# Performance work log

Hardware: AMD Instinct MI355X
Metric: run time of the kernel (lower is better)

## Reference

```python
import jax, jax.numpy as jnp
import numpy as np

B = 4096      # batch
D_IN = 512    # input_dim
D = 256       # d_model
T = 424       # n_targets
L = 6         # num_layers
EPS = 1e-5    # torch LayerNorm default


def _ln(x, g, b):
    m = jnp.mean(x, axis=-1, keepdims=True)
    v = jnp.var(x, axis=-1, keepdims=True)
    return (x - m) * jax.lax.rsqrt(v + EPS) * g + b


def setup_inputs() -> dict:
    key = jax.random.key(0)
    ks = iter(jax.random.split(key, 32))
    r = lambda shape, s=0.05: jax.random.normal(next(ks), shape, dtype=jnp.float32) * s
    return {
        'x': jax.random.normal(next(ks), (B, D_IN), dtype=jnp.float32),
        'proj_W': r((4, D // 4, D_IN)), 'proj_b': r((4, D // 4)),
        'attn_in_W': r((L, 3 * D, D)), 'attn_in_b': r((L, 3 * D)),
        'attn_out_W': r((L, D, D)), 'attn_out_b': r((L, D)),
        'ln_g': jnp.ones((L, D), jnp.float32), 'ln_b': jnp.zeros((L, D), jnp.float32),
        'ff_W1': r((L, 4 * D, D)), 'ff_b1': r((L, 4 * D)),
        'ff_W2': r((L, D, 4 * D)), 'ff_b2': r((L, D)),
        'cross_in_W': r((3 * D, D)), 'cross_in_b': r((3 * D,)),
        'cross_out_W': r((D, D)), 'cross_out_b': r((D,)),
        'tp_W1': r((T, D // 2, D)), 'tp_b1': r((T, D // 2)),
        'tp_ln_g': jnp.ones((T, D // 2), jnp.float32), 'tp_ln_b': jnp.zeros((T, D // 2), jnp.float32),
        'tp_W2': r((T, D // 4, D // 2)), 'tp_b2': r((T, D // 4)),
        'tp_W3': r((T, D // 4)), 'tp_b3': r((T,)),
    }


def reference(x, proj_W, proj_b, attn_in_W, attn_in_b, attn_out_W, attn_out_b,
              ln_g, ln_b, ff_W1, ff_b1, ff_W2, ff_b2,
              cross_in_W, cross_in_b, cross_out_W, cross_out_b,
              tp_W1, tp_b1, tp_ln_g, tp_ln_b, tp_W2, tp_b2, tp_W3, tp_b3):
    # 4 feature projections -> concat == reshape of stacked einsum  [B, 4, D/4] -> [B, D]
    h = jnp.einsum('bd,pkd->bpk', x, proj_W) + proj_b
    h = h.reshape(h.shape[0], D)

    # 6 transformer blocks on seq_len=1: softmax over a single key == 1, so
    # MHA(x,x,x) reduces exactly to out_proj(v_proj(x)); dropout = identity (eval).
    for i in range(L):
        Wv, bv = attn_in_W[i, 2 * D:], attn_in_b[i, 2 * D:]
        attn = (h @ Wv.T + bv) @ attn_out_W[i].T + attn_out_b[i]
        h = _ln(h + attn, ln_g[i], ln_b[i])          # same norm instance reused
        ff = jax.nn.gelu(h @ ff_W1[i].T + ff_b1[i], approximate=False) @ ff_W2[i].T + ff_b2[i]
        h = _ln(h + ff, ln_g[i], ln_b[i])

    # cross-target attention, also seq_len=1 -> v/out projections only
    Wv, bv = cross_in_W[2 * D:], cross_in_b[2 * D:]
    h = h + ((h @ Wv.T + bv) @ cross_out_W.T + cross_out_b)

    # 424 per-target MLP heads, batched as grouped GEMMs
    t = jnp.einsum('bd,tkd->btk', h, tp_W1) + tp_b1          # [B, T, 128]
    t = jax.nn.relu(_ln(t, tp_ln_g, tp_ln_b))
    t = jax.nn.relu(jnp.einsum('btk,tmk->btm', t, tp_W2) + tp_b2)  # [B, T, 64]
    out = jnp.einsum('btm,tm->bt', t, tp_W3) + tp_b3         # [B, T]
    return out
```

## Files before the change

### kernel.cpp

```cpp
#include <hip/hip_runtime.h>
#include <stdint.h>
#include <utility>
#include <type_traits>

using bf16x8 = __attribute__((ext_vector_type(8))) short;
using f32x4  = __attribute__((ext_vector_type(4))) float;

__device__ __forceinline__ f32x4 mfma16(bf16x8 a, bf16x8 b, f32x4 c) {
  return __builtin_amdgcn_mfma_f32_16x16x32_bf16(a, b, c, 0, 0, 0);
}

__device__ __forceinline__ unsigned short f2b_rne(float f) {
  union { float f; unsigned u; } v; v.f = f;
  unsigned r = v.u + 0x7fffu + ((v.u >> 16) & 1u);
  return (unsigned short)(r >> 16);
}

__device__ __forceinline__ void gload16(const void* g, void* l) {
  __builtin_amdgcn_global_load_lds(
      (const __attribute__((address_space(1))) void*)g,
      (__attribute__((address_space(3))) void*)l, 16, 0, 0);
}

template<int N> __device__ __forceinline__ void vmwait() {
  if constexpr (N <= 0)      asm volatile("s_waitcnt vmcnt(0)" ::: "memory");
  else if constexpr (N == 4) asm volatile("s_waitcnt vmcnt(4)" ::: "memory");
  else                       asm volatile("s_waitcnt vmcnt(8)" ::: "memory");
}

template<class F, int... Is>
__device__ __forceinline__ void sfor_impl(F&& f, std::integer_sequence<int, Is...>) {
  (f(std::integral_constant<int, Is>{}), ...);
}
template<int N, class F>
__device__ __forceinline__ void sfor(F&& f) {
  sfor_impl(static_cast<F&&>(f), std::make_integer_sequence<int, N>{});
}

__device__ __forceinline__ void stage_tile(const unsigned short* __restrict__ W, int K,
                                           int col0, int kt, char* slot, int lane) {
#pragma unroll
  for (int i = 0; i < 4; ++i) {
    const int chunk = i * 64 + lane;
    const int ci = chunk >> 4, kc = chunk & 15;
    const unsigned short* src = W + (size_t)(col0 + ci) * K + kt * 128
                                + (((kc * 16) ^ ((ci & 7) << 4)) >> 1);
    gload16(src, slot + i * 1024);
  }
}

template<int NCG, int NKT, int AS, int K>
__device__ __forceinline__ void gemm_pipe(const unsigned short* __restrict__ W, int c0,
                                          const char* __restrict__ abuf,
                                          char* __restrict__ ring, int lane,
                                          f32x4 (&acc)[NCG]) {
  const int r = lane & 15, hi16 = (lane >> 4) << 4;
  const int swz = (r & 7) << 4;
  constexpr int TILES = NCG * NKT;
  stage_tile(W, K, c0, 0, ring, lane);
  if constexpr (TILES > 1)
    stage_tile(W, K, c0 + (1 % NCG) * 16, 1 / NCG, ring + 4096, lane);
  bf16x8 areg[4];
  sfor<TILES>([&](auto tc) {
    constexpr int t = tc.value;
    constexpr int kt = t / NCG, cg = t % NCG;
    vmwait<((t + 2 <= TILES) ? 4 : 0)>();
    __builtin_amdgcn_sched_barrier(0);
    if constexpr (t + 2 < TILES) {
      constexpr int t2 = t + 2;
      stage_tile(W, K, c0 + (t2 % NCG) * 16, t2 / NCG, ring + (t2 % 3) * 4096, lane);
    }
    const char* slot = ring + (t % 3) * 4096;
#pragma unroll
    for (int ksl = 0; ksl < 4; ++ksl) {
      if constexpr (cg == 0)
        areg[ksl] = *reinterpret_cast<const bf16x8*>(
            abuf + r * AS + ((kt * 256 + ksl * 64 + hi16) ^ swz));
      const bf16x8 b = *reinterpret_cast<const bf16x8*>(
          slot + r * 256 + ((ksl * 64 + hi16) ^ swz));
      acc[cg] = mfma16(areg[ksl], b, acc[cg]);
    }
  });
}

__global__ void f2b_kernel(const float* __restrict__ s, unsigned short* __restrict__ d, int n4) {
  int i = blockIdx.x * 256 + threadIdx.x;
  if (i >= n4) return;
  float4 v = reinterpret_cast<const float4*>(s)[i];
  ushort4 o;
  o.x = f2b_rne(v.x); o.y = f2b_rne(v.y); o.z = f2b_rne(v.z); o.w = f2b_rne(v.w);
  reinterpret_cast<ushort4*>(d)[i] = o;
}

__global__ __launch_bounds__(256) void compose_attn(
    const float* __restrict__ aiW, const float* __restrict__ aib,
    const float* __restrict__ aoW, const float* __restrict__ aob,
    const float* __restrict__ ciW, const float* __restrict__ cib,
    const float* __restrict__ coW, const float* __restrict__ cob,
    unsigned short* __restrict__ wEff, float* __restrict__ bEff) {
  const int mat = blockIdx.y;
  const float* Wo = (mat < 6) ? aoW + (size_t)mat * 65536 : coW;
  const float* Wv = (mat < 6) ? aiW + (size_t)mat * 196608 + 131072 : ciW + 131072;
  const float* bv = (mat < 6) ? aib + mat * 768 + 512 : cib + 512;
  const float* bo = (mat < 6) ? aob + mat * 256 : cob;
  unsigned short* Wd = wEff + (size_t)mat * 65536;
  const int m = blockIdx.x * 16 + (threadIdx.x >> 4);
  const int k0 = (threadIdx.x & 15) * 16;
  float c[16] = {};
  for (int j = 0; j < 256; ++j) {
    const float a = Wo[m * 256 + j];
    const float* Br = Wv + j * 256 + k0;
#pragma unroll
    for (int kk = 0; kk < 16; ++kk) c[kk] = fmaf(a, Br[kk], c[kk]);
  }
#pragma unroll
  for (int kk = 0; kk < 16; ++kk) Wd[m * 256 + k0 + kk] = f2b_rne(c[kk]);
  if (blockIdx.x == 0) {
    const int mm = threadIdx.x;
    float s = 0.f;
    for (int j = 0; j < 256; ++j) s = fmaf(Wo[mm * 256 + j], bv[j], s);
    bEff[mat * 256 + mm] = s + bo[mm];
  }
}

__global__ __launch_bounds__(512, 2) void trunk_fused(
    const unsigned short* __restrict__ xb, const unsigned short* __restrict__ pWb,
    const float* __restrict__ projb,
    const unsigned short* __restrict__ wEff, const float* __restrict__ bEff,
    const unsigned short* __restrict__ f1Wb, const float* __restrict__ f1b,
    const unsigned short* __restrict__ f2Wb, const float* __restrict__ f2bp,
    const float* __restrict__ lng, const float* __restrict__ lnb,
    unsigned short* __restrict__ hbf) {
  __shared__ char hbuf[16 * 512];
  __shared__ char gbuf[16 * 2048];
  __shared__ char ringbuf[8 * 12288];
  __shared__ float red[2][16][8];
  const int tid = threadIdx.x, wid = tid >> 6, lane = tid & 63;
  const int r = lane & 15, hi = lane >> 4;
  const int swz = (r & 7) << 4;
  const int row0 = blockIdx.x << 4;
  const int colb = wid * 32;
  char* ring = ringbuf + wid * 12288;

#pragma unroll
  for (int i = 0; i < 2; ++i) {
    const int id = tid + i * 512, row = id >> 6, c8 = id & 63;
    bf16x8 v = *reinterpret_cast<const bf16x8*>(xb + (size_t)(row0 + row) * 512 + c8 * 8);
    *reinterpret_cast<bf16x8*>(gbuf + row * 1024 + ((c8 * 16) ^ ((row & 7) << 4))) = v;
  }
  __syncthreads();

  f32x4 hreg[2];

  auto store_hb = [&]() {
#pragma unroll
    for (int cf = 0; cf < 2; ++cf) {
      const int cb = (colb + cf * 16 + r) * 2;
#pragma unroll
      for (int j = 0; j < 4; ++j) {
        const int row = hi * 4 + j;
        *reinterpret_cast<unsigned short*>(hbuf + row * 512 + (cb ^ ((row & 7) << 4))) =
            f2b_rne(hreg[cf][j]);
      }
    }
  };

  auto ln_apply = [&](float gm0, float gm1, float bb0, float bb1) {
    float sum[4], sq[4];
#pragma unroll
    for (int j = 0; j < 4; ++j) {
      const float v0 = hreg[0][j], v1 = hreg[1][j];
      sum[j] = v0 + v1; sq[j] = v0 * v0 + v1 * v1;
    }
#pragma unroll
    for (int m = 1; m < 16; m <<= 1)
#pragma unroll
      for (int j = 0; j < 4; ++j) {
        sum[j] += __shfl_xor(sum[j], m, 64);
        sq[j]  += __shfl_xor(sq[j],  m, 64);
      }
    if (r == 0)
#pragma unroll
      for (int j = 0; j < 4; ++j) {
        red[0][hi * 4 + j][wid] = sum[j];
        red[1][hi * 4 + j][wid] = sq[j];
      }
    __syncthreads();
#pragma unroll
    for (int j = 0; j < 4; ++j) {
      const int row = hi * 4 + j;
      f32x4 p0 = *reinterpret_cast<const f32x4*>(&red[0][row][0]);
      f32x4 p1 = *reinterpret_cast<const f32x4*>(&red[0][row][4]);
      f32x4 q0 = *reinterpret_cast<const f32x4*>(&red[1][row][0]);
      f32x4 q1 = *reinterpret_cast<const f32x4*>(&red[1][row][4]);
      const float ts = p0[0]+p0[1]+p0[2]+p0[3]+p1[0]+p1[1]+p1[2]+p1[3];
      const float tq = q0[0]+q0[1]+q0[2]+q0[3]+q1[0]+q1[1]+q1[2]+q1[3];
      const float mean = ts * (1.f / 256.f);
      const float rstd = rsqrtf(tq * (1.f / 256.f) - mean * mean + 1e-5f);
      hreg[0][j] = (hreg[0][j] - mean) * rstd * gm0 + bb0;
      hreg[1][j] = (hreg[1][j] - mean) * rstd * gm1 + bb1;
    }
  };

  {
    f32x4 acc[2] = {};
    gemm_pipe<2, 4, 1024, 512>(pWb, colb, gbuf, ring, lane, acc);
    const float bv0 = projb[colb + r], bv1 = projb[colb + 16 + r];
#pragma unroll
    for (int j = 0; j < 4; ++j) { hreg[0][j] = acc[0][j] + bv0; hreg[1][j] = acc[1][j] + bv1; }
  }
  store_hb();
  __syncthreads();

  for (int L = 0; L < 6; ++L) {
    const float gm0 = lng[L * 256 + colb + r],      gm1 = lng[L * 256 + colb + 16 + r];
    const float bb0 = lnb[L * 256 + colb + r],      bb1 = lnb[L * 256 + colb + 16 + r];
    {
      f32x4 acc[2] = {};
      gemm_pipe<2, 2, 512, 256>(wEff + (size_t)L * 65536, colb, hbuf, ring, lane, acc);
      const float be0 = bEff[L * 256 + colb + r], be1 = bEff[L * 256 + colb + 16 + r];
#pragma unroll
      for (int j = 0; j < 4; ++j) { hreg[0][j] += acc[0][j] + be0; hreg[1][j] += acc[1][j] + be1; }
    }
    ln_apply(gm0, gm1, bb0, bb1);
    store_hb();
    __syncthreads();
    {
      f32x4 accf[8] = {};
      gemm_pipe<8, 2, 512, 256>(f1Wb + (size_t)L * 262144, wid * 128, hbuf, ring, lane, accf);
#pragma unroll
      for (int cf = 0; cf < 8; ++cf) {
        const int colw = wid * 128 + cf * 16 + r;
        const float bv = f1b[L * 1024 + colw];
        const int cb = colw * 2;
#pragma unroll
        for (int j = 0; j < 4; ++j) {
          float y = accf[cf][j] + bv;
          y = 0.5f * y * (1.f + erff(y * 0.70710678118654752f));
          const int row = hi * 4 + j;
          *reinterpret_cast<unsigned short*>(gbuf + row * 2048 + (cb ^ ((row & 7) << 4))) = f2b_rne(y);
        }
      }
    }
    __syncthreads();
    {
      f32x4 acc[2] = {};
      gemm_pipe<2, 8, 2048, 1024>(f2Wb + (size_t)L * 262144, colb, gbuf, ring, lane, acc);
      const float be0 = f2bp[L * 256 + colb + r], be1 = f2bp[L * 256 + colb + 16 + r];
#pragma unroll
      for (int j = 0; j < 4; ++j) { hreg[0][j] += acc[0][j] + be0; hreg[1][j] += acc[1][j] + be1; }
    }
    ln_apply(gm0, gm1, bb0, bb1);
    store_hb();
    __syncthreads();
  }

  {
    f32x4 acc[2] = {};
    gemm_pipe<2, 2, 512, 256>(wEff + 6ull * 65536, colb, hbuf, ring, lane, acc);
    const float be0 = bEff[1536 + colb + r], be1 = bEff[1536 + colb + 16 + r];
#pragma unroll
    for (int j = 0; j < 4; ++j) { hreg[0][j] += acc[0][j] + be0; hreg[1][j] += acc[1][j] + be1; }
  }
#pragma unroll
  for (int cf = 0; cf < 2; ++cf)
#pragma unroll
    for (int j = 0; j < 4; ++j)
      hbf[(size_t)(row0 + hi * 4 + j) * 256 + colb + cf * 16 + r] = f2b_rne(hreg[cf][j]);
}

__global__ __launch_bounds__(512, 2) void phase_d2(
    const unsigned short* __restrict__ hbf, const unsigned short* __restrict__ w1b,
    const float* __restrict__ b1, const float* __restrict__ lng, const float* __restrict__ lnb,
    const unsigned short* __restrict__ w2b, const float* __restrict__ b2,
    const float* __restrict__ w3, const float* __restrict__ b3,
    float* __restrict__ out) {
  __shared__ char sm[149504];
  const int tid = threadIdx.x, wid = tid >> 6, lane = tid & 63;
  const int r = lane & 15, hi = lane >> 4;
  const int sw = (r & 7) << 4;
  const int t = blockIdx.y;

  const unsigned short* w1t = w1b + (size_t)t * 32768;
  const unsigned short* w2t = w2b + (size_t)t * 8192;
#pragma unroll
  for (int i = 0; i < 8; ++i) {
    const int id = tid + i * 512;
    const int c = id >> 5, s = id & 31;
    bf16x8 v = *reinterpret_cast<const bf16x8*>(w1t + c * 256 + s * 8);
    *reinterpret_cast<bf16x8*>(sm + c * 512 + ((s * 16) ^ ((c & 7) << 4))) = v;
  }
#pragma unroll
  for (int i = 0; i < 2; ++i) {
    const int id = tid + i * 512;
    const int c = id >> 4, s = id & 15;
    bf16x8 v = *reinterpret_cast<const bf16x8*>(w2t + c * 128 + s * 8);
    *reinterpret_cast<bf16x8*>(sm + 65536 + c * 256 + ((s * 16) ^ ((c & 7) << 4))) = v;
  }
  {
    float v;
    if (tid < 128)      v = b1 [t * 128 + tid];
    else if (tid < 256) v = lng[t * 128 + tid - 128];
    else if (tid < 384) v = lnb[t * 128 + tid - 256];
    else if (tid < 448) v = b2 [t * 64  + tid - 384];
    else                v = w3 [t * 64  + tid - 448];
    reinterpret_cast<float*>(sm + 81920)[tid] = v;
  }
  __syncthreads();

  const float* cb1 = reinterpret_cast<const float*>(sm + 81920);
  const float* cg  = cb1 + 128;
  const float* cbe = cb1 + 256;
  const float* cb2 = cb1 + 384;
  const float* cw3 = cb1 + 448;
  char* t1w = sm + 83968 + wid * 8192;
  const float b3t = b3[t];
  const int token_b0 = blockIdx.x * 1024;

  for (int tile = 0; tile < 2; ++tile) {
    const int B0 = token_b0 + tile * 512 + wid * 64;

    f32x4 acc1[8][4] = {};
    bf16x8 bc[4], bn[4];
#pragma unroll
    for (int bf = 0; bf < 4; ++bf)
      bc[bf] = *reinterpret_cast<const bf16x8*>(hbf + (size_t)(B0 + bf * 16 + r) * 256 + hi * 8);
#pragma unroll
    for (int ks = 0; ks < 8; ++ks) {
      bf16x8 a[8];
#pragma unroll
      for (int cf = 0; cf < 8; ++cf)
        a[cf] = *reinterpret_cast<const bf16x8*>(sm + (cf * 16 + r) * 512 + ((ks * 64 + hi * 16) ^ sw));
      if (ks < 7) {
#pragma unroll
        for (int bf = 0; bf < 4; ++bf)
          bn[bf] = *reinterpret_cast<const bf16x8*>(hbf + (size_t)(B0 + bf * 16 + r) * 256 + (ks + 1) * 32 + hi * 8);
      }
#pragma unroll
      for (int cf = 0; cf < 8; ++cf)
#pragma unroll
        for (int bf = 0; bf < 4; ++bf)
          acc1[cf][bf] = mfma16(a[cf], bc[bf], acc1[cf][bf]);
#pragma unroll
      for (int bf = 0; bf < 4; ++bf) bc[bf] = bn[bf];
    }

#pragma unroll
    for (int cf = 0; cf < 8; ++cf) {
      f32x4 b1v = *reinterpret_cast<const f32x4*>(cb1 + cf * 16 + hi * 4);
#pragma unroll
      for (int bf = 0; bf < 4; ++bf) acc1[cf][bf] += b1v;
    }

    float mu[4], rsd[4];
#pragma unroll
    for (int bf = 0; bf < 4; ++bf) {
      float s = 0.f, s2 = 0.f;
#pragma unroll
      for (int cf = 0; cf < 8; ++cf)
#pragma unroll
        for (int j = 0; j < 4; ++j) { float v = acc1[cf][bf][j]; s += v; s2 += v * v; }
      s  += __shfl_xor(s, 16, 64);  s  += __shfl_xor(s, 32, 64);
      s2 += __shfl_xor(s2, 16, 64); s2 += __shfl_xor(s2, 32, 64);
      const float m = s * (1.f / 128.f);
      mu[bf] = m;
      rsd[bf] = rsqrtf(s2 * (1.f / 128.f) - m * m + 1e-5f);
    }

    f32x4 acc2[4][4] = {};
#pragma unroll
    for (int half = 0; half < 2; ++half) {
#pragma unroll
      for (int cf = 0; cf < 8; ++cf) {
        f32x4 gv = *reinterpret_cast<const f32x4*>(cg  + cf * 16 + hi * 4);
        f32x4 bv = *reinterpret_cast<const f32x4*>(cbe + cf * 16 + hi * 4);
#pragma unroll
        for (int bl = 0; bl < 2; ++bl) {
          const int bf = half * 2 + bl;
          unsigned o01, o23;
          {
            float y0 = fmaxf((acc1[cf][bf][0] - mu[bf]) * rsd[bf] * gv[0] + bv[0], 0.f);
            float y1 = fmaxf((acc1[cf][bf][1] - mu[bf]) * rsd[bf] * gv[1] + bv[1], 0.f);
            float y2 = fmaxf((acc1[cf][bf][2] - mu[bf]) * rsd[bf] * gv[2] + bv[2], 0.f);
            float y3 = fmaxf((acc1[cf][bf][3] - mu[bf]) * rsd[bf] * gv[3] + bv[3], 0.f);
            o01 = (unsigned)f2b_rne(y0) | ((unsigned)f2b_rne(y1) << 16);
            o23 = (unsigned)f2b_rne(y2) | ((unsigned)f2b_rne(y3) << 16);
          }
          uint2 pk; pk.x = o01; pk.y = o23;
          *reinterpret_cast<uint2*>(t1w + (bl * 16 + r) * 256 + ((cf * 32 + hi * 8) ^ sw)) = pk;
        }
      }
#pragma unroll
      for (int ks = 0; ks < 4; ++ks) {
        bf16x8 a2[4];
#pragma unroll
        for (int cf2 = 0; cf2 < 4; ++cf2)
          a2[cf2] = *reinterpret_cast<const bf16x8*>(sm + 65536 + (cf2 * 16 + r) * 256 + ((ks * 64 + hi * 16) ^ sw));
#pragma unroll
        for (int bl = 0; bl < 2; ++bl) {
          bf16x8 bb = *reinterpret_cast<const bf16x8*>(t1w + (bl * 16 + r) * 256 + ((ks * 64 + hi * 16) ^ sw));
#pragma unroll
          for (int cf2 = 0; cf2 < 4; ++cf2)
            acc2[cf2][half * 2 + bl] = mfma16(a2[cf2], bb, acc2[cf2][half * 2 + bl]);
        }
      }
    }

    float s[4] = {0.f, 0.f, 0.f, 0.f};
#pragma unroll
    for (int cf2 = 0; cf2 < 4; ++cf2) {
      f32x4 b2v = *reinterpret_cast<const f32x4*>(cb2 + cf2 * 16 + hi * 4);
      f32x4 w3v = *reinterpret_cast<const f32x4*>(cw3 + cf2 * 16 + hi * 4);
#pragma unroll
      for (int bf = 0; bf < 4; ++bf)
#pragma unroll
        for (int j = 0; j < 4; ++j)
          s[bf] += fmaxf(acc2[cf2][bf][j] + b2v[j], 0.f) * w3v[j];
    }
#pragma unroll
    for (int bf = 0; bf < 4; ++bf) {
      s[bf] += __shfl_xor(s[bf], 16, 64);
      s[bf] += __shfl_xor(s[bf], 32, 64);
      if (hi == 0) out[(size_t)(B0 + bf * 16 + r) * 424 + t] = s[bf] + b3t;
    }
  }
}

extern "C" void kernel_launch(void* const* d_in, const int* in_sizes, int n_in,
                              void* d_out, int out_size, void* d_ws, size_t ws_size,
                              hipStream_t stream) {
  const float* x     = (const float*)d_in[0];
  const float* projW = (const float*)d_in[1];
  const float* projb = (const float*)d_in[2];
  const float* aiW   = (const float*)d_in[3];
  const float* aib   = (const float*)d_in[4];
  const float* aoW   = (const float*)d_in[5];
  const float* aob   = (const float*)d_in[6];
  const float* lng   = (const float*)d_in[7];
  const float* lnbp  = (const float*)d_in[8];
  const float* f1W   = (const float*)d_in[9];
  const float* f1b   = (const float*)d_in[10];
  const float* f2W   = (const float*)d_in[11];
  const float* f2bp  = (const float*)d_in[12];
  const float* ciW   = (const float*)d_in[13];
  const float* cib   = (const float*)d_in[14];
  const float* coW   = (const float*)d_in[15];
  const float* cob   = (const float*)d_in[16];
  const float* tpW1  = (const float*)d_in[17];
  const float* tpb1  = (const float*)d_in[18];
  const float* tplng = (const float*)d_in[19];
  const float* tplnb = (const float*)d_in[20];
  const float* tpW2  = (const float*)d_in[21];
  const float* tpb2  = (const float*)d_in[22];
  const float* tpW3  = (const float*)d_in[23];
  const float* tpb3  = (const float*)d_in[24];
  float* out = (float*)d_out;

  char* ws = (char*)d_ws;
  size_t off = 0;
  auto alloc = [&](size_t n) { char* p = ws + off; off = (off + n + 255) & ~(size_t)255; return p; };
  unsigned short* xb   = (unsigned short*)alloc(4096ull * 512 * 2);
  unsigned short* pWb  = (unsigned short*)alloc(256ull * 512 * 2);
  unsigned short* f1Wb = (unsigned short*)alloc(6ull * 1024 * 256 * 2);
  unsigned short* f2Wb = (unsigned short*)alloc(6ull * 256 * 1024 * 2);
  unsigned short* W1b  = (unsigned short*)alloc(424ull * 128 * 256 * 2);
  unsigned short* W2b  = (unsigned short*)alloc(424ull * 64 * 128 * 2);
  unsigned short* wEff = (unsigned short*)alloc(7ull * 256 * 256 * 2);
  float*          bEff = (float*)alloc(7ull * 256 * 4);
  unsigned short* hbf  = (unsigned short*)alloc(4096ull * 256 * 2);

  auto conv = [&](const float* s, unsigned short* d, size_t n) {
    int n4 = (int)(n >> 2);
    f2b_kernel<<<dim3((n4 + 255) / 256), dim3(256), 0, stream>>>(s, d, n4);
  };
  compose_attn<<<dim3(16, 7), dim3(256), 0, stream>>>(aiW, aib, aoW, aob, ciW, cib, coW, cob, wEff, bEff);
  conv(x, xb, 4096ull * 512);
  conv(projW, pWb, 256ull * 512);
  conv(f1W, f1Wb, 6ull * 1024 * 256);
  conv(f2W, f2Wb, 6ull * 256 * 1024);
  conv(tpW1, W1b, 424ull * 128 * 256);
  conv(tpW2, W2b, 424ull * 64 * 128);

  trunk_fused<<<dim3(256), dim3(512), 0, stream>>>(
      xb, pWb, projb, wEff, bEff, f1Wb, f1b, f2Wb, f2bp, lng, lnbp, hbf);

  phase_d2<<<dim3(4, 424), dim3(512), 0, stream>>>(hbf, W1b, tpb1, tplng, tplnb, W2b, tpb2, tpW3, tpb3, out);
}
```

Baseline: 523.6 us.

## Shrink head kernel LDS/tiles, exchange LN output via shuffles, raise occupancy

The per-target head kernel now gives each workgroup 256 tokens (32 per wave) instead of 1024, over a 1D grid of 6784 blocks laid out so consecutive blocks pair up on the same target. The LDS staging of W2 and of the per-wave t1 scratch is dropped. The second GEMM's B fragments are rebuilt with cross-lane shuffles from packed registers, and W2, b2 and w3 are read directly from global memory. This lowers shared memory to about 67KB and launch bounds to 4 blocks per CU to raise occupancy. The cost is that W1 is reloaded into LDS four times more often per target, and there are more shuffle instructions.

```diff
diff --git a/kernel.cpp b/kernel.cpp
--- a/kernel.cpp
+++ b/kernel.cpp
@@ -5,6 +5,7 @@
 
 using bf16x8 = __attribute__((ext_vector_type(8))) short;
 using f32x4  = __attribute__((ext_vector_type(4))) float;
+using u32x4  = __attribute__((ext_vector_type(4))) unsigned;
 
 __device__ __forceinline__ f32x4 mfma16(bf16x8 a, bf16x8 b, f32x4 c) {
   return __builtin_amdgcn_mfma_f32_16x16x32_bf16(a, b, c, 0, 0, 0);
@@ -137,7 +138,6 @@
   __shared__ float red[2][16][8];
   const int tid = threadIdx.x, wid = tid >> 6, lane = tid & 63;
   const int r = lane & 15, hi = lane >> 4;
-  const int swz = (r & 7) << 4;
   const int row0 = blockIdx.x << 4;
   const int colb = wid * 32;
   char* ring = ringbuf + wid * 12288;
@@ -269,20 +269,24 @@
       hbf[(size_t)(row0 + hi * 4 + j) * 256 + colb + cf * 16 + r] = f2b_rne(hreg[cf][j]);
 }
 
-__global__ __launch_bounds__(512, 2) void phase_d2(
+__global__ __launch_bounds__(512, 4) void phase_d4(
     const unsigned short* __restrict__ hbf, const unsigned short* __restrict__ w1b,
     const float* __restrict__ b1, const float* __restrict__ lng, const float* __restrict__ lnb,
     const unsigned short* __restrict__ w2b, const float* __restrict__ b2,
     const float* __restrict__ w3, const float* __restrict__ b3,
     float* __restrict__ out) {
-  __shared__ char sm[149504];
+  __shared__ char sm[65536 + 1536];
   const int tid = threadIdx.x, wid = tid >> 6, lane = tid & 63;
   const int r = lane & 15, hi = lane >> 4;
   const int sw = (r & 7) << 4;
-  const int t = blockIdx.y;
+
+  const int wg = blockIdx.x;
+  const int pp = wg / 848, rem = wg % 848;
+  const int t = rem >> 1;
+  const int part = pp * 2 + (rem & 1);
+  const int B0 = part * 256 + wid * 32;
 
   const unsigned short* w1t = w1b + (size_t)t * 32768;
-  const unsigned short* w2t = w2b + (size_t)t * 8192;
 #pragma unroll
   for (int i = 0; i < 8; ++i) {
     const int id = tid + i * 512;
@@ -290,40 +294,24 @@
     bf16x8 v = *reinterpret_cast<const bf16x8*>(w1t + c * 256 + s * 8);
     *reinterpret_cast<bf16x8*>(sm + c * 512 + ((s * 16) ^ ((c & 7) << 4))) = v;
   }
-#pragma unroll
-  for (int i = 0; i < 2; ++i) {
-    const int id = tid + i * 512;
-    const int c = id >> 4, s = id & 15;
-    bf16x8 v = *reinterpret_cast<const bf16x8*>(w2t + c * 128 + s * 8);
-    *reinterpret_cast<bf16x8*>(sm + 65536 + c * 256 + ((s * 16) ^ ((c & 7) << 4))) = v;
-  }
-  {
+  if (tid < 384) {
     float v;
     if (tid < 128)      v = b1 [t * 128 + tid];
     else if (tid < 256) v = lng[t * 128 + tid - 128];
-    else if (tid < 384) v = lnb[t * 128 + tid - 256];
-    else if (tid < 448) v = b2 [t * 64  + tid - 384];
-    else                v = w3 [t * 64  + tid - 448];
-    reinterpret_cast<float*>(sm + 81920)[tid] = v;
+    else                v = lnb[t * 128 + tid - 256];
+    reinterpret_cast<float*>(sm + 65536)[tid] = v;
   }
   __syncthreads();
 
-  const float* cb1 = reinterpret_cast<const float*>(sm + 81920);
+  const float* cb1 = reinterpret_cast<const float*>(sm + 65536);
   const float* cg  = cb1 + 128;
   const float* cbe = cb1 + 256;
-  const float* cb2 = cb1 + 384;
-  const float* cw3 = cb1 + 448;
-  char* t1w = sm + 83968 + wid * 8192;
-  const float b3t = b3[t];
-  const int token_b0 = blockIdx.x * 1024;
-
-  for (int tile = 0; tile < 2; ++tile) {
-    const int B0 = token_b0 + tile * 512 + wid * 64;
-
-    f32x4 acc1[8][4] = {};
-    bf16x8 bc[4], bn[4];
-#pragma unroll
-    for (int bf = 0; bf < 4; ++bf)
+
+  f32x4 acc1[8][2] = {};
+  {
+    bf16x8 bc[2], bn[2];
+#pragma unroll
+    for (int bf = 0; bf < 2; ++bf)
       bc[bf] = *reinterpret_cast<const bf16x8*>(hbf + (size_t)(B0 + bf * 16 + r) * 256 + hi * 8);
 #pragma unroll
     for (int ks = 0; ks < 8; ++ks) {
@@ -333,96 +321,108 @@
         a[cf] = *reinterpret_cast<const bf16x8*>(sm + (cf * 16 + r) * 512 + ((ks * 64 + hi * 16) ^ sw));
       if (ks < 7) {
 #pragma unroll
-        for (int bf = 0; bf < 4; ++bf)
+        for (int bf = 0; bf < 2; ++bf)
           bn[bf] = *reinterpret_cast<const bf16x8*>(hbf + (size_t)(B0 + bf * 16 + r) * 256 + (ks + 1) * 32 + hi * 8);
       }
 #pragma unroll
       for (int cf = 0; cf < 8; ++cf)
 #pragma unroll
-        for (int bf = 0; bf < 4; ++bf)
+        for (int bf = 0; bf < 2; ++bf)
           acc1[cf][bf] = mfma16(a[cf], bc[bf], acc1[cf][bf]);
 #pragma unroll
-      for (int bf = 0; bf < 4; ++bf) bc[bf] = bn[bf];
-    }
-
-#pragma unroll
-    for (int cf = 0; cf < 8; ++cf) {
-      f32x4 b1v = *reinterpret_cast<const f32x4*>(cb1 + cf * 16 + hi * 4);
-#pragma unroll
-      for (int bf = 0; bf < 4; ++bf) acc1[cf][bf] += b1v;
-    }
-
-    float mu[4], rsd[4];
-#pragma unroll
-    for (int bf = 0; bf < 4; ++bf) {
-      float s = 0.f, s2 = 0.f;
-#pragma unroll
-      for (int cf = 0; cf < 8; ++cf)
-#pragma unroll
-        for (int j = 0; j < 4; ++j) { float v = acc1[cf][bf][j]; s += v; s2 += v * v; }
-      s  += __shfl_xor(s, 16, 64);  s  += __shfl_xor(s, 32, 64);
-      s2 += __shfl_xor(s2, 16, 64); s2 += __shfl_xor(s2, 32, 64);
-      const float m = s * (1.f / 128.f);
-      mu[bf] = m;
-      rsd[bf] = rsqrtf(s2 * (1.f / 128.f) - m * m + 1e-5f);
-    }
-
-    f32x4 acc2[4][4] = {};
-#pragma unroll
-    for (int half = 0; half < 2; ++half) {
-#pragma unroll
-      for (int cf = 0; cf < 8; ++cf) {
-        f32x4 gv = *reinterpret_cast<const f32x4*>(cg  + cf * 16 + hi * 4);
-        f32x4 bv = *reinterpret_cast<const f32x4*>(cbe + cf * 16 + hi * 4);
-#pragma unroll
-        for (int bl = 0; bl < 2; ++bl) {
-          const int bf = half * 2 + bl;
-          unsigned o01, o23;
-          {
-            float y0 = fmaxf((acc1[cf][bf][0] - mu[bf]) * rsd[bf] * gv[0] + bv[0], 0.f);
-            float y1 = fmaxf((acc1[cf][bf][1] - mu[bf]) * rsd[bf] * gv[1] + bv[1], 0.f);
-            float y2 = fmaxf((acc1[cf][bf][2] - mu[bf]) * rsd[bf] * gv[2] + bv[2], 0.f);
-            float y3 = fmaxf((acc1[cf][bf][3] - mu[bf]) * rsd[bf] * gv[3] + bv[3], 0.f);
-            o01 = (unsigned)f2b_rne(y0) | ((unsigned)f2b_rne(y1) << 16);
-            o23 = (unsigned)f2b_rne(y2) | ((unsigned)f2b_rne(y3) << 16);
-          }
-          uint2 pk; pk.x = o01; pk.y = o23;
-          *reinterpret_cast<uint2*>(t1w + (bl * 16 + r) * 256 + ((cf * 32 + hi * 8) ^ sw)) = pk;
-        }
-      }
-#pragma unroll
-      for (int ks = 0; ks < 4; ++ks) {
-        bf16x8 a2[4];
-#pragma unroll
-        for (int cf2 = 0; cf2 < 4; ++cf2)
-          a2[cf2] = *reinterpret_cast<const bf16x8*>(sm + 65536 + (cf2 * 16 + r) * 256 + ((ks * 64 + hi * 16) ^ sw));
-#pragma unroll
-        for (int bl = 0; bl < 2; ++bl) {
-          bf16x8 bb = *reinterpret_cast<const bf16x8*>(t1w + (bl * 16 + r) * 256 + ((ks * 64 + hi * 16) ^ sw));
-#pragma unroll
-          for (int cf2 = 0; cf2 < 4; ++cf2)
-            acc2[cf2][half * 2 + bl] = mfma16(a2[cf2], bb, acc2[cf2][half * 2 + bl]);
-        }
-      }
-    }
-
-    float s[4] = {0.f, 0.f, 0.f, 0.f};
-#pragma unroll
-    for (int cf2 = 0; cf2 < 4; ++cf2) {
-      f32x4 b2v = *reinterpret_cast<const f32x4*>(cb2 + cf2 * 16 + hi * 4);
-      f32x4 w3v = *reinterpret_cast<const f32x4*>(cw3 + cf2 * 16 + hi * 4);
-#pragma unroll
-      for (int bf = 0; bf < 4; ++bf)
-#pragma unroll
-        for (int j = 0; j < 4; ++j)
-          s[bf] += fmaxf(acc2[cf2][bf][j] + b2v[j], 0.f) * w3v[j];
-    }
-#pragma unroll
-    for (int bf = 0; bf < 4; ++bf) {
-      s[bf] += __shfl_xor(s[bf], 16, 64);
-      s[bf] += __shfl_xor(s[bf], 32, 64);
-      if (hi == 0) out[(size_t)(B0 + bf * 16 + r) * 424 + t] = s[bf] + b3t;
-    }
+      for (int bf = 0; bf < 2; ++bf) bc[bf] = bn[bf];
+    }
+  }
+
+#pragma unroll
+  for (int cf = 0; cf < 8; ++cf) {
+    f32x4 b1v = *reinterpret_cast<const f32x4*>(cb1 + cf * 16 + hi * 4);
+#pragma unroll
+    for (int bf = 0; bf < 2; ++bf) acc1[cf][bf] += b1v;
+  }
+  float mu[2], rsd[2];
+#pragma unroll
+  for (int bf = 0; bf < 2; ++bf) {
+    float s = 0.f, s2 = 0.f;
+#pragma unroll
+    for (int cf = 0; cf < 8; ++cf)
+#pragma unroll
+      for (int j = 0; j < 4; ++j) { float v = acc1[cf][bf][j]; s += v; s2 += v * v; }
+    s  += __shfl_xor(s, 16, 64);  s  += __shfl_xor(s, 32, 64);
+    s2 += __shfl_xor(s2, 16, 64); s2 += __shfl_xor(s2, 32, 64);
+    const float m = s * (1.f / 128.f);
+    mu[bf] = m;
+    rsd[bf] = rsqrtf(s2 * (1.f / 128.f) - m * m + 1e-5f);
+  }
+
+  unsigned pk01[8][2], pk23[8][2];
+#pragma unroll
+  for (int cf = 0; cf < 8; ++cf) {
+    f32x4 gv = *reinterpret_cast<const f32x4*>(cg  + cf * 16 + hi * 4);
+    f32x4 bv = *reinterpret_cast<const f32x4*>(cbe + cf * 16 + hi * 4);
+#pragma unroll
+    for (int bf = 0; bf < 2; ++bf) {
+      f32x4 a4, d4;
+#pragma unroll
+      for (int j = 0; j < 4; ++j) { a4[j] = gv[j] * rsd[bf]; d4[j] = bv[j] - mu[bf] * a4[j]; }
+      float y0 = fmaxf(acc1[cf][bf][0] * a4[0] + d4[0], 0.f);
+      float y1 = fmaxf(acc1[cf][bf][1] * a4[1] + d4[1], 0.f);
+      float y2 = fmaxf(acc1[cf][bf][2] * a4[2] + d4[2], 0.f);
+      float y3 = fmaxf(acc1[cf][bf][3] * a4[3] + d4[3], 0.f);
+      pk01[cf][bf] = (unsigned)f2b_rne(y0) | ((unsigned)f2b_rne(y1) << 16);
+      pk23[cf][bf] = (unsigned)f2b_rne(y2) | ((unsigned)f2b_rne(y3) << 16);
+    }
+  }
+
+  const unsigned short* w2t = w2b + (size_t)t * 8192;
+  f32x4 acc2[4][2] = {};
+  const int srcA = r + 32 * (lane >> 4 & 1);
+  const bool lohalf = (hi < 2);
+#pragma unroll
+  for (int ks = 0; ks < 4; ++ks) {
+    bf16x8 a2[4];
+#pragma unroll
+    for (int cf2 = 0; cf2 < 4; ++cf2)
+      a2[cf2] = *reinterpret_cast<const bf16x8*>(w2t + (cf2 * 16 + r) * 128 + ks * 32 + hi * 8);
+#pragma unroll
+    for (int bf = 0; bf < 2; ++bf) {
+      const unsigned s0 = __shfl(pk01[2 * ks][bf], srcA, 64);
+      const unsigned s1 = __shfl(pk23[2 * ks][bf], srcA, 64);
+      const unsigned s2 = __shfl(pk01[2 * ks][bf], srcA + 16, 64);
+      const unsigned s3 = __shfl(pk23[2 * ks][bf], srcA + 16, 64);
+      const unsigned t0 = __shfl(pk01[2 * ks + 1][bf], srcA, 64);
+      const unsigned t1v = __shfl(pk23[2 * ks + 1][bf], srcA, 64);
+      const unsigned t2 = __shfl(pk01[2 * ks + 1][bf], srcA + 16, 64);
+      const unsigned t3 = __shfl(pk23[2 * ks + 1][bf], srcA + 16, 64);
+      u32x4 bu;
+      bu[0] = lohalf ? s0 : t0;
+      bu[1] = lohalf ? s1 : t1v;
+      bu[2] = lohalf ? s2 : t2;
+      bu[3] = lohalf ? s3 : t3;
+      const bf16x8 bfrag = __builtin_bit_cast(bf16x8, bu);
+#pragma unroll
+      for (int cf2 = 0; cf2 < 4; ++cf2)
+        acc2[cf2][bf] = mfma16(a2[cf2], bfrag, acc2[cf2][bf]);
+    }
+  }
+
+  const float b3t = b3[t];
+  float s[2] = {0.f, 0.f};
+#pragma unroll
+  for (int cf2 = 0; cf2 < 4; ++cf2) {
+    f32x4 b2v = *reinterpret_cast<const f32x4*>(b2 + t * 64 + cf2 * 16 + hi * 4);
+    f32x4 w3v = *reinterpret_cast<const f32x4*>(w3 + t * 64 + cf2 * 16 + hi * 4);
+#pragma unroll
+    for (int bf = 0; bf < 2; ++bf)
+#pragma unroll
+      for (int j = 0; j < 4; ++j)
+        s[bf] += fmaxf(acc2[cf2][bf][j] + b2v[j], 0.f) * w3v[j];
+  }
+#pragma unroll
+  for (int bf = 0; bf < 2; ++bf) {
+    s[bf] += __shfl_xor(s[bf], 16, 64);
+    s[bf] += __shfl_xor(s[bf], 32, 64);
+    if (hi == 0) out[(size_t)(B0 + bf * 16 + r) * 424 + t] = s[bf] + b3t;
   }
 }
 
@@ -484,5 +484,5 @@
   trunk_fused<<<dim3(256), dim3(512), 0, stream>>>(
       xb, pWb, projb, wEff, bEff, f1Wb, f1b, f2Wb, f2bp, lng, lnbp, hbf);
 
-  phase_d2<<<dim3(4, 424), dim3(512), 0, stream>>>(hbf, W1b, tpb1, tplng, tplnb, W2b, tpb2, tpW3, tpb3, out);
-}
+  phase_d4<<<dim3(6784), dim3(512), 0, stream>>>(hbf, W1b, tpb1, tplng, tplnb, W2b, tpb2, tpW3, tpb3, out);
+}
```

After: 593.9 us, median of 2. 1.13x slower.
